# Kernel optimization log

Measured on AMD Instinct MI355X. Metric: run time of the kernel, lower is better.

## Reference

```python
import jax, jax.numpy as jnp
import numpy as np

D, H, W = 20, 18, 18      # f_dim = (20, 72//4, 72//4); depth == feature_ch
PI = 3.14159              # constant used in the torch module


def make_grid():
    # matches make_coordinate_grid_3d: normalized coords in [-1, 1]
    x = 2.0 * jnp.arange(W, dtype=jnp.float32) / (W - 1) - 1.0
    y = 2.0 * jnp.arange(H, dtype=jnp.float32) / (H - 1) - 1.0
    z = 2.0 * jnp.arange(D, dtype=jnp.float32) / (D - 1) - 1.0
    xx = jnp.broadcast_to(x[None, None, :], (D, H, W))
    yy = jnp.broadcast_to(y[None, :, None], (D, H, W))
    zz = jnp.broadcast_to(z[:, None, None], (D, H, W))
    grid_xy = jnp.stack([xx, yy], axis=-1)   # (D,H,W,2), order (x, y)
    return grid_xy, zz


def trilinear_sample(vol, grid):
    # vol: (D,H,W); grid: (D,H,W,3) with (x,y,z) in [-1,1]
    # F.grid_sample defaults: mode='bilinear' (trilinear), padding='zeros', align_corners=False
    ix = ((grid[..., 0] + 1.0) * W - 1.0) * 0.5
    iy = ((grid[..., 1] + 1.0) * H - 1.0) * 0.5
    iz = ((grid[..., 2] + 1.0) * D - 1.0) * 0.5
    x0, y0, z0 = jnp.floor(ix), jnp.floor(iy), jnp.floor(iz)
    wx, wy, wz = ix - x0, iy - y0, iz - z0
    vflat = vol.reshape(-1)
    out = jnp.zeros_like(ix)
    for cz in (0, 1):
        for cy in (0, 1):
            for cx in (0, 1):
                xi = x0 + cx
                yi = y0 + cy
                zi = z0 + cz
                w = ((wx if cx else 1.0 - wx)
                     * (wy if cy else 1.0 - wy)
                     * (wz if cz else 1.0 - wz))
                valid = ((xi >= 0) & (xi < W) & (yi >= 0) & (yi < H)
                         & (zi >= 0) & (zi < D))
                xi_c = jnp.clip(xi, 0, W - 1).astype(jnp.int32)
                yi_c = jnp.clip(yi, 0, H - 1).astype(jnp.int32)
                zi_c = jnp.clip(zi, 0, D - 1).astype(jnp.int32)
                idx = (zi_c * H + yi_c) * W + xi_c
                out = out + jnp.where(valid, w * vflat[idx], 0.0)
    return out


def setup_inputs() -> dict:
    key = jax.random.key(0)
    ks = jax.random.split(key, 10)
    B, P, F = 4096, 256, 20
    s = 0.05
    return {
        "feature_map": jax.random.normal(ks[0], (B, F, H, W), jnp.float32),
        "para_code": jax.random.normal(ks[1], (B, P), jnp.float32),
        "W1": jax.random.normal(ks[2], (P, P), jnp.float32) * s,
        "b1": jax.random.normal(ks[3], (P,), jnp.float32) * s,
        "Ws": jax.random.normal(ks[4], (P, F), jnp.float32) * s,
        "bs": jax.random.normal(ks[5], (F,), jnp.float32) * s,
        "Wr": jax.random.normal(ks[6], (P, F), jnp.float32) * s,
        "br": jax.random.normal(ks[7], (F,), jnp.float32) * s,
        "Wt": jax.random.normal(ks[8], (P, 2 * F), jnp.float32) * s,
        "bt": jax.random.normal(ks[9], (2 * F,), jnp.float32) * s,
    }


def reference(feature_map, para_code, W1, b1, Ws, bs, Wr, br, Wt, bt):
    B, F = feature_map.shape[0], feature_map.shape[1]  # F == D == 20
    grid_xy, grid_z = make_grid()
    h = jax.nn.relu(para_code @ W1 + b1)                     # commn_linear
    scale = jax.nn.sigmoid(h @ Ws + bs) * 2.0                # (B,F)
    angle = jnp.tanh(h @ Wr + br) * PI                       # (B,F)
    trans = jnp.tanh(h @ Wt + bt).reshape(B, F, 2)           # (B,F,2)
    c, s = jnp.cos(angle), jnp.sin(angle)
    rot = jnp.stack([jnp.stack([c, -s], -1),
                     jnp.stack([s, c], -1)], -2)             # (B,F,2,2)
    g = grid_xy.reshape(F, H * W, 2)                          # depth == feature_ch
    # per-channel affine: rotate, scale, translate each grid point
    tg = jnp.einsum('bfij,fpj->bfpi', rot, g)                 # (B,F,HW,2)
    tg = tg * scale[:, :, None, None] + trans[:, :, None, :]
    full_grid = jnp.concatenate(
        [tg.reshape(B, F, H, W, 2),
         jnp.broadcast_to(grid_z, (B, F, H, W))[..., None]], axis=-1)
    return jax.vmap(trilinear_sample)(feature_map, full_grid)
```

## Files before the change

### kernel.cpp

```cpp
#include <hip/hip_runtime.h>

#define PI_F 3.14159f

__global__ __launch_bounds__(256) void params_kernel(
    const float* __restrict__ pc, const float* __restrict__ W1, const float* __restrict__ b1,
    const float* __restrict__ Ws, const float* __restrict__ bs,
    const float* __restrict__ Wr, const float* __restrict__ br,
    const float* __restrict__ Wt, const float* __restrict__ bt,
    float* __restrict__ params)
{
    __shared__ float para[8][256];
    __shared__ float hbuf[8][260];
    __shared__ float raw[8][80];

    const int t  = threadIdx.x;
    const int b0 = blockIdx.x * 8;

    #pragma unroll
    for (int g = 0; g < 8; ++g) para[g][t] = pc[(size_t)(b0 + g) * 256 + t];
    __syncthreads();

    float acc[8];
    #pragma unroll
    for (int g = 0; g < 8; ++g) acc[g] = b1[t];
    for (int k = 0; k < 256; ++k) {
        float w = W1[k * 256 + t];
        #pragma unroll
        for (int g = 0; g < 8; ++g) acc[g] = fmaf(para[g][k], w, acc[g]);
    }
    #pragma unroll
    for (int g = 0; g < 8; ++g) hbuf[g][t] = fmaxf(acc[g], 0.0f);
    __syncthreads();

    for (int task = t; task < 640; task += 256) {
        int g   = task / 80;
        int col = task - g * 80;
        const float* Wcol;
        float bias;
        int stride;
        if (col < 20)      { Wcol = Ws + col;        bias = bs[col];      stride = 20; }
        else if (col < 40) { Wcol = Wr + (col - 20); bias = br[col - 20]; stride = 20; }
        else               { Wcol = Wt + (col - 40); bias = bt[col - 40]; stride = 40; }
        float a = bias;
        for (int k = 0; k < 256; ++k) a = fmaf(hbuf[g][k], Wcol[k * stride], a);
        raw[g][col] = a;
    }
    __syncthreads();

    for (int task = t; task < 160; task += 256) {
        int g = task / 20;
        int f = task - g * 20;
        float sc  = 2.0f / (1.0f + expf(-raw[g][f]));
        float ang = PI_F * tanhf(raw[g][20 + f]);
        float tx  = tanhf(raw[g][40 + 2 * f]);
        float ty  = tanhf(raw[g][40 + 2 * f + 1]);
        float c = cosf(ang), s = sinf(ang);
        float* o = params + ((size_t)(b0 + g) * 20 + f) * 8;
        o[0] = sc * c;  o[1] = -sc * s;
        o[2] = sc * s;  o[3] = sc * c;
        o[4] = tx;      o[5] = ty;
        o[6] = 0.0f;    o[7] = 0.0f;
    }
}

__global__ __launch_bounds__(256) void sample_kernel(
    const float* __restrict__ fmap, const float* __restrict__ params,
    float* __restrict__ out)
{
    __shared__ __align__(16) float vol[6480];
    __shared__ float prm[160];

    const int b = blockIdx.x;
    const int t = threadIdx.x;

    const float4* src4 = (const float4*)(fmap + (size_t)b * 6480);
    float4* vol4 = (float4*)vol;
    for (int i = t; i < 1620; i += 256) vol4[i] = src4[i];
    if (t < 160) prm[t] = params[(size_t)b * 160 + t];
    __syncthreads();

    float* outb = out + (size_t)b * 6480;

    for (int p = t; p < 6480; p += 256) {
        int d   = p / 324;
        int rem = p - d * 324;
        int hy  = rem / 18;
        int wxi = rem - hy * 18;

        float X = wxi * (2.0f / 17.0f) - 1.0f;
        float Y = hy  * (2.0f / 17.0f) - 1.0f;

        const float* pr = prm + d * 8;
        float gx = fmaf(pr[0], X, fmaf(pr[1], Y, pr[4]));
        float gy = fmaf(pr[2], X, fmaf(pr[3], Y, pr[5]));

        float ix = fmaf(gx, 9.0f, 8.5f);
        float iy = fmaf(gy, 9.0f, 8.5f);
        float iz = fmaf((float)d, 20.0f / 19.0f, -0.5f);

        float fx = floorf(ix), fy = floorf(iy), fz = floorf(iz);
        float u1 = ix - fx, v1 = iy - fy, w1 = iz - fz;
        float u0 = 1.0f - u1, v0 = 1.0f - v1, w0 = 1.0f - w1;

        int x0 = (int)fx, y0 = (int)fy, z0 = (int)fz;
        int x1 = x0 + 1,  y1 = y0 + 1,  z1 = z0 + 1;

        float ax0 = ((unsigned)x0 < 18u) ? u0 : 0.0f;
        float ax1 = ((unsigned)x1 < 18u) ? u1 : 0.0f;
        float ay0 = ((unsigned)y0 < 18u) ? v0 : 0.0f;
        float ay1 = ((unsigned)y1 < 18u) ? v1 : 0.0f;
        float az0 = ((unsigned)z0 < 20u) ? w0 : 0.0f;
        float az1 = ((unsigned)z1 < 20u) ? w1 : 0.0f;

        int xc0 = min(max(x0, 0), 17), xc1 = min(max(x1, 0), 17);
        int yc0 = min(max(y0, 0), 17), yc1 = min(max(y1, 0), 17);
        int zc0 = min(max(z0, 0), 19), zc1 = min(max(z1, 0), 19);

        int zb0 = zc0 * 324, zb1 = zc1 * 324;
        int yb0 = yc0 * 18,  yb1 = yc1 * 18;

        float v000 = vol[zb0 + yb0 + xc0], v001 = vol[zb0 + yb0 + xc1];
        float v010 = vol[zb0 + yb1 + xc0], v011 = vol[zb0 + yb1 + xc1];
        float v100 = vol[zb1 + yb0 + xc0], v101 = vol[zb1 + yb0 + xc1];
        float v110 = vol[zb1 + yb1 + xc0], v111 = vol[zb1 + yb1 + xc1];

        float r0 = fmaf(fmaf(v001, ax1, v000 * ax0), ay0,
                        fmaf(v011, ax1, v010 * ax0) * ay1);
        float r1 = fmaf(fmaf(v101, ax1, v100 * ax0), ay0,
                        fmaf(v111, ax1, v110 * ax0) * ay1);

        outb[p] = fmaf(r0, az0, r1 * az1);
    }
}

extern "C" void kernel_launch(void* const* d_in, const int* in_sizes, int n_in,
                              void* d_out, int out_size, void* d_ws, size_t ws_size,
                              hipStream_t stream)
{
    const float* fmap = (const float*)d_in[0];
    const float* pc   = (const float*)d_in[1];
    const float* W1   = (const float*)d_in[2];
    const float* b1   = (const float*)d_in[3];
    const float* Ws   = (const float*)d_in[4];
    const float* bs   = (const float*)d_in[5];
    const float* Wr   = (const float*)d_in[6];
    const float* br   = (const float*)d_in[7];
    const float* Wt   = (const float*)d_in[8];
    const float* bt   = (const float*)d_in[9];
    float* out    = (float*)d_out;
    float* params = (float*)d_ws;

    const int B = in_sizes[0] / (20 * 18 * 18);

    params_kernel<<<B / 8, 256, 0, stream>>>(pc, W1, b1, Ws, bs, Wr, br, Wt, bt, params);
    sample_kernel<<<B, 256, 0, stream>>>(fmap, params, out);
}
```

Before: 274.9 us.

## Use zero-padded shared volume, fold index scaling into params, unroll depth at compile time

The sampler now keeps each volume in a zero-padded 20x20 per-slice shared layout. This removes all bounds checks and weight masking, since out-of-range taps read zeros. The grid-to-index scaling is folded into the affine params in params_kernel. Each thread owns one (y,x) position and loops over the 20 depth slices through a template recursion with compile-time z weights. This skips the boundary z slice and drops the division and mod math. The costs are a zero-fill pass, scalar strided global loads in place of float4 loads, 384-thread blocks with 60 idle threads, more shared memory per block, and clamping at 19 that relies on the padding.

```diff
diff --git a/kernel.cpp b/kernel.cpp
--- a/kernel.cpp
+++ b/kernel.cpp
@@ -56,81 +56,110 @@
         float ty  = tanhf(raw[g][40 + 2 * f + 1]);
         float c = cosf(ang), s = sinf(ang);
         float* o = params + ((size_t)(b0 + g) * 20 + f) * 8;
-        o[0] = sc * c;  o[1] = -sc * s;
-        o[2] = sc * s;  o[3] = sc * c;
-        o[4] = tx;      o[5] = ty;
-        o[6] = 0.0f;    o[7] = 0.0f;
+        o[0] = 9.0f * sc * c;  o[1] = -9.0f * sc * s;  o[2] = fmaf(9.0f, tx, 9.5f);
+        o[3] = 9.0f * sc * s;  o[4] =  9.0f * sc * c;  o[5] = fmaf(9.0f, ty, 9.5f);
+        o[6] = 0.0f;           o[7] = 0.0f;
     }
 }
 
-__global__ __launch_bounds__(256) void sample_kernel(
+template<int D>
+__device__ __forceinline__ void slice(const float* __restrict__ pb,
+                                      const float* vol,
+                                      float X, float Y,
+                                      float* __restrict__ ob)
+{
+    constexpr int   Z0  = (D == 0) ? -1 : (40 * D - 19) / 38;
+    constexpr float W1v = ((40.0f * D - 19.0f) - 38.0f * (float)Z0) / 38.0f;
+    constexpr float W0v = 1.0f - W1v;
+    constexpr bool  V0  = (Z0 >= 0);
+    constexpr bool  V1  = (Z0 + 1 <= 19);
+
+    float4 pA = *(const float4*)(pb + D * 8);
+    float2 pB = *(const float2*)(pb + D * 8 + 4);
+
+    float ix = fmaf(pA.x, X, fmaf(pA.y, Y, pA.z));
+    float iy = fmaf(pA.w, X, fmaf(pB.x, Y, pB.y));
+
+    float fx = floorf(ix), fy = floorf(iy);
+    float u1 = ix - fx, v1 = iy - fy;
+    float u0 = 1.0f - u1, v0 = 1.0f - v1;
+
+    int x0 = (int)fx, y0 = (int)fy;
+    int xc0 = min(max(x0, 0), 19), xc1 = min(max(x0 + 1, 0), 19);
+    int yc0 = min(max(y0, 0), 19), yc1 = min(max(y0 + 1, 0), 19);
+
+    int a00 = yc0 * 20 + xc0, a01 = yc0 * 20 + xc1;
+    int a10 = yc1 * 20 + xc0, a11 = yc1 * 20 + xc1;
+
+    float r0 = 0.0f, r1 = 0.0f;
+    if constexpr (V0) {
+        const float* s = vol + Z0 * 400;
+        float t00 = s[a00], t01 = s[a01], t10 = s[a10], t11 = s[a11];
+        r0 = fmaf(fmaf(t01, u1, t00 * u0), v0, fmaf(t11, u1, t10 * u0) * v1);
+    }
+    if constexpr (V1) {
+        const float* s = vol + (Z0 + 1) * 400;
+        float t00 = s[a00], t01 = s[a01], t10 = s[a10], t11 = s[a11];
+        r1 = fmaf(fmaf(t01, u1, t00 * u0), v0, fmaf(t11, u1, t10 * u0) * v1);
+    }
+
+    float r;
+    if constexpr (!V0)      r = r1 * W1v;
+    else if constexpr (!V1) r = r0 * W0v;
+    else                    r = fmaf(r0, W0v, r1 * W1v);
+
+    ob[D * 324] = r;
+}
+
+template<int D>
+struct Run {
+    static __device__ __forceinline__ void go(const float* __restrict__ pb,
+                                              const float* vol,
+                                              float X, float Y,
+                                              float* __restrict__ ob) {
+        slice<D>(pb, vol, X, Y, ob);
+        Run<D + 1>::go(pb, vol, X, Y, ob);
+    }
+};
+template<>
+struct Run<20> {
+    static __device__ __forceinline__ void go(const float*, const float*,
+                                              float, float, float*) {}
+};
+
+__global__ __launch_bounds__(384) void sample_kernel(
     const float* __restrict__ fmap, const float* __restrict__ params,
     float* __restrict__ out)
 {
-    __shared__ __align__(16) float vol[6480];
-    __shared__ float prm[160];
+    __shared__ __align__(16) float vol[8000];
 
     const int b = blockIdx.x;
     const int t = threadIdx.x;
 
-    const float4* src4 = (const float4*)(fmap + (size_t)b * 6480);
-    float4* vol4 = (float4*)vol;
-    for (int i = t; i < 1620; i += 256) vol4[i] = src4[i];
-    if (t < 160) prm[t] = params[(size_t)b * 160 + t];
+    float4* v4 = (float4*)vol;
+    for (int i = t; i < 2000; i += 384) v4[i] = make_float4(0.f, 0.f, 0.f, 0.f);
     __syncthreads();
 
-    float* outb = out + (size_t)b * 6480;
+    const float* fb = fmap + (size_t)b * 6480;
+    int yy = 0, xx = 0;
+    if (t < 324) {
+        yy = t / 18;
+        xx = t - yy * 18;
+        const int w = (yy + 1) * 20 + (xx + 1);
+        #pragma unroll
+        for (int dz = 0; dz < 20; ++dz)
+            vol[dz * 400 + w] = fb[dz * 324 + t];
+    }
+    __syncthreads();
 
-    for (int p = t; p < 6480; p += 256) {
-        int d   = p / 324;
-        int rem = p - d * 324;
-        int hy  = rem / 18;
-        int wxi = rem - hy * 18;
+    if (t >= 324) return;
 
-        float X = wxi * (2.0f / 17.0f) - 1.0f;
-        float Y = hy  * (2.0f / 17.0f) - 1.0f;
+    const float X = xx * (2.0f / 17.0f) - 1.0f;
+    const float Y = yy * (2.0f / 17.0f) - 1.0f;
+    const float* pb = params + (size_t)b * 160;
+    float* ob = out + (size_t)b * 6480 + t;
 
-        const float* pr = prm + d * 8;
-        float gx = fmaf(pr[0], X, fmaf(pr[1], Y, pr[4]));
-        float gy = fmaf(pr[2], X, fmaf(pr[3], Y, pr[5]));
-
-        float ix = fmaf(gx, 9.0f, 8.5f);
-        float iy = fmaf(gy, 9.0f, 8.5f);
-        float iz = fmaf((float)d, 20.0f / 19.0f, -0.5f);
-
-        float fx = floorf(ix), fy = floorf(iy), fz = floorf(iz);
-        float u1 = ix - fx, v1 = iy - fy, w1 = iz - fz;
-        float u0 = 1.0f - u1, v0 = 1.0f - v1, w0 = 1.0f - w1;
-
-        int x0 = (int)fx, y0 = (int)fy, z0 = (int)fz;
-        int x1 = x0 + 1,  y1 = y0 + 1,  z1 = z0 + 1;
-
-        float ax0 = ((unsigned)x0 < 18u) ? u0 : 0.0f;
-        float ax1 = ((unsigned)x1 < 18u) ? u1 : 0.0f;
-        float ay0 = ((unsigned)y0 < 18u) ? v0 : 0.0f;
-        float ay1 = ((unsigned)y1 < 18u) ? v1 : 0.0f;
-        float az0 = ((unsigned)z0 < 20u) ? w0 : 0.0f;
-        float az1 = ((unsigned)z1 < 20u) ? w1 : 0.0f;
-
-        int xc0 = min(max(x0, 0), 17), xc1 = min(max(x1, 0), 17);
-        int yc0 = min(max(y0, 0), 17), yc1 = min(max(y1, 0), 17);
-        int zc0 = min(max(z0, 0), 19), zc1 = min(max(z1, 0), 19);
-
-        int zb0 = zc0 * 324, zb1 = zc1 * 324;
-        int yb0 = yc0 * 18,  yb1 = yc1 * 18;
-
-        float v000 = vol[zb0 + yb0 + xc0], v001 = vol[zb0 + yb0 + xc1];
-        float v010 = vol[zb0 + yb1 + xc0], v011 = vol[zb0 + yb1 + xc1];
-        float v100 = vol[zb1 + yb0 + xc0], v101 = vol[zb1 + yb0 + xc1];
-        float v110 = vol[zb1 + yb1 + xc0], v111 = vol[zb1 + yb1 + xc1];
-
-        float r0 = fmaf(fmaf(v001, ax1, v000 * ax0), ay0,
-                        fmaf(v011, ax1, v010 * ax0) * ay1);
-        float r1 = fmaf(fmaf(v101, ax1, v100 * ax0), ay0,
-                        fmaf(v111, ax1, v110 * ax0) * ay1);
-
-        outb[p] = fmaf(r0, az0, r1 * az1);
-    }
+    Run<0>::go(pb, vol, X, Y, ob);
 }
 
 extern "C" void kernel_launch(void* const* d_in, const int* in_sizes, int n_in,
@@ -153,5 +182,5 @@
     const int B = in_sizes[0] / (20 * 18 * 18);
 
     params_kernel<<<B / 8, 256, 0, stream>>>(pc, W1, b1, Ws, bs, Wr, br, Wt, bt, params);
-    sample_kernel<<<B, 256, 0, stream>>>(fmap, params, out);
+    sample_kernel<<<B, 384, 0, stream>>>(fmap, params, out);
 }
```

New measurement: 262.0 us. -4.7%, faster.
